# Kernel tuning notes

Hardware: AMD Instinct MI355X
Metric: run time of the kernel (lower is better)

## Reference

```python
import jax, jax.numpy as jnp
import numpy as np
import math

DIM = 1024
D_FF = 1024
B = 128


def setup_inputs() -> dict:
    key = jax.random.key(0)
    ks = jax.random.split(key, 13)
    s = 1.0 / math.sqrt(DIM)
    sf = 1.0 / math.sqrt(D_FF)
    return {
        "x": jax.random.normal(ks[0], (B, DIM), dtype=jnp.float32),
        "Wq": jax.random.uniform(ks[1], (DIM, DIM), jnp.float32, -s, s),
        "bq": jax.random.uniform(ks[2], (DIM,), jnp.float32, -s, s),
        "Wk": jax.random.uniform(ks[3], (DIM, DIM), jnp.float32, -s, s),
        "bk": jax.random.uniform(ks[4], (DIM,), jnp.float32, -s, s),
        "Wv": jax.random.uniform(ks[5], (DIM, DIM), jnp.float32, -s, s),
        "bv": jax.random.uniform(ks[6], (DIM,), jnp.float32, -s, s),
        "Wo": jax.random.uniform(ks[7], (DIM, DIM), jnp.float32, -s, s),
        "bo": jax.random.uniform(ks[8], (DIM,), jnp.float32, -s, s),
        "W1": jax.random.uniform(ks[9], (D_FF, DIM), jnp.float32, -s, s),
        "b1": jax.random.uniform(ks[10], (D_FF,), jnp.float32, -s, s),
        "W2": jax.random.uniform(ks[11], (DIM, D_FF), jnp.float32, -sf, sf),
        "b2": jax.random.uniform(ks[12], (DIM,), jnp.float32, -sf, sf),
    }


def reference(x, Wq, bq, Wk, bk, Wv, bv, Wo, bo, W1, b1, W2, b2):
    # Attention (eval mode: dropout is identity)
    q = x @ Wq.T + bq                      # [B, D]
    k = x @ Wk.T + bk                      # [B, D]
    v = x @ Wv.T + bv                      # [B, D]
    inv_sqrt_dk = 1.0 / math.sqrt(DIM)
    # per-sample outer product: weights[b, i, j] = q[b,i] * k[b,j] / sqrt(d_k)
    weights = (q[:, :, None] * k[:, None, :]) * inv_sqrt_dk  # [B, D, D]
    nw = jax.nn.softmax(weights, axis=-1)                    # [B, D, D]
    attn_out = jnp.einsum('bij,bj->bi', nw, v)               # [B, D]
    attn_out = attn_out @ Wo.T + bo
    # residual 1
    x2 = x + attn_out
    # FFN
    h = jax.nn.relu(x2 @ W1.T + b1)        # [B, d_ff]
    ff = h @ W2.T + b2                     # [B, D]
    out = x2 + ff
    return (out, nw)
```

## Files before the change

### kernel.cpp

```cpp
#include <hip/hip_runtime.h>

#define DIM   1024
#define BATCH 128
#define MAT   (BATCH*DIM)
#define NROWS MAT
#define DS    32

typedef float f4n __attribute__((ext_vector_type(4)));

#define Q_AT  28672
#define A_WO  28672
#define B_WO  47104
#define A_W1  54272
#define B_W1  72704
#define A_W2  79872
#define B_W2  98304
#define MBASE 105472

struct Params {
  const float *x,*Wq,*bq,*Wk,*bk,*Wv,*bv,*Wo,*bo,*W1,*b1,*W2,*b2;
  float *out,*nw;
  float *q,*k,*v,*araw,*x2,*h,*rinv,*P;
};

template<bool USE_RINV>
__device__ __forceinline__ void write_row(const Params& p, int row, int lane)
{
  const int b = row >> 10;
  const float4* __restrict__ k4 = (const float4*)(p.k + ((size_t)b<<10));
  const float4 k0 = k4[lane      ], k1 = k4[lane +  64];
  const float4 k2 = k4[lane + 128], k3 = k4[lane + 192];
  const float c = p.q[row] * 0.03125f;
  f4n* o = (f4n*)(p.nw + ((size_t)row<<10));

  float e[16];
  e[ 0]=__expf(c*k0.x); e[ 1]=__expf(c*k0.y); e[ 2]=__expf(c*k0.z); e[ 3]=__expf(c*k0.w);
  e[ 4]=__expf(c*k1.x); e[ 5]=__expf(c*k1.y); e[ 6]=__expf(c*k1.z); e[ 7]=__expf(c*k1.w);
  e[ 8]=__expf(c*k2.x); e[ 9]=__expf(c*k2.y); e[10]=__expf(c*k2.z); e[11]=__expf(c*k2.w);
  e[12]=__expf(c*k3.x); e[13]=__expf(c*k3.y); e[14]=__expf(c*k3.z); e[15]=__expf(c*k3.w);

  float rinv;
  if (USE_RINV) {
    rinv = p.rinv[row];
  } else {
    float sum = 0.f;
#pragma unroll
    for (int i=0;i<16;++i) sum += e[i];
#pragma unroll
    for (int off=32; off>=1; off>>=1) sum += __shfl_xor(sum, off);
    rinv = 1.f/sum;
  }
#pragma unroll
  for (int t=0;t<4;++t) {
    f4n st;
    st.x = e[4*t+0]*rinv; st.y = e[4*t+1]*rinv;
    st.z = e[4*t+2]*rinv; st.w = e[4*t+3]*rinv;
    __builtin_nontemporal_store(st, &o[lane + 64*t]);
  }
}

template<bool USE_RINV>
__device__ __forceinline__ void write_strided(const Params& p, int w, int NW,
                                              int base, int cap, int lane)
{
#pragma unroll 1
  for (int row = base + w; row < cap; row += NW)
    write_row<USE_RINV>(p, row, lane);
}

__device__ __forceinline__ void ar_rows(const Params& p, int r0, int r1, int lane)
{
  int bcur = -1;
  float4 kr[4], vr[4];
#pragma unroll 1
  for (int row = r0; row < r1; ++row) {
    const int b = row >> 10;
    if (b != bcur) {
      bcur = b;
      const float4* __restrict__ k4 = (const float4*)(p.k + ((size_t)b<<10));
      const float4* __restrict__ v4 = (const float4*)(p.v + ((size_t)b<<10));
#pragma unroll
      for (int t=0;t<4;++t) { kr[t] = k4[lane + 64*t]; vr[t] = v4[lane + 64*t]; }
    }
    const float c = p.q[row] * 0.03125f;
    float sum=0.f, dot=0.f;
#pragma unroll
    for (int t=0;t<4;++t) {
      const float4 kk = kr[t];
      const float4 vv = vr[t];
      float ex = __expf(c*kk.x), ey = __expf(c*kk.y);
      float ez = __expf(c*kk.z), ew = __expf(c*kk.w);
      sum += (ex+ey)+(ez+ew);
      dot += ex*vv.x + ey*vv.y + ez*vv.z + ew*vv.w;
    }
#pragma unroll
    for (int off=32; off>=1; off>>=1) {
      sum += __shfl_xor(sum, off);
      dot += __shfl_xor(dot, off);
    }
    const float rinv = 1.f/sum;
    if (lane==0) { p.araw[row] = dot*rinv; p.rinv[row] = rinv; }
  }
}

__device__ __forceinline__ void gemm_tile(
    const float* __restrict__ X, const float* __restrict__ W,
    float* __restrict__ Pout, int n0, int k0, int KC,
    float* xt, float* wt)
{
  const int tid = threadIdx.x;
  const int tn = tid & 15, tb = tid >> 4;
  const int b_base = tb*8, n_base = tn*4;
  float acc[8][4];
#pragma unroll
  for (int i=0;i<8;++i)
#pragma unroll
    for (int j=0;j<4;++j) acc[i][j]=0.f;

  for (int s=0; s<KC/DS; ++s) {
    const int kk = k0 + s*DS;
#pragma unroll
    for (int r=0;r<4;++r) {
      const int row = (tid>>3) + 32*r;
      const int c0  = (tid&7)*4;
      const float4 vv = *(const float4*)(X + (size_t)row*DIM + kk + c0);
      xt[(c0+0)*132+row]=vv.x; xt[(c0+1)*132+row]=vv.y;
      xt[(c0+2)*132+row]=vv.z; xt[(c0+3)*132+row]=vv.w;
    }
#pragma unroll
    for (int r=0;r<2;++r) {
      const int row = (tid>>3) + 32*r;
      const int c0  = (tid&7)*4;
      const f4n vv = __builtin_nontemporal_load(
          (const f4n*)(W + (size_t)(n0+row)*DIM + kk + c0));
      wt[(c0+0)*68+row]=vv.x; wt[(c0+1)*68+row]=vv.y;
      wt[(c0+2)*68+row]=vv.z; wt[(c0+3)*68+row]=vv.w;
    }
    __syncthreads();
#pragma unroll 4
    for (int d=0; d<DS; ++d) {
      const float4 xa0 = *(const float4*)&xt[d*132 + b_base];
      const float4 xa1 = *(const float4*)&xt[d*132 + b_base + 4];
      const float4 wa  = *(const float4*)&wt[d*68  + n_base];
      const float xr[8] = {xa0.x,xa0.y,xa0.z,xa0.w, xa1.x,xa1.y,xa1.z,xa1.w};
      const float wr[4] = {wa.x,wa.y,wa.z,wa.w};
#pragma unroll
      for (int bb=0;bb<8;++bb)
#pragma unroll
        for (int nn=0;nn<4;++nn) acc[bb][nn] += xr[bb]*wr[nn];
    }
    __syncthreads();
  }
#pragma unroll
  for (int bb=0;bb<8;++bb) {
    const float4 st = make_float4(acc[bb][0],acc[bb][1],acc[bb][2],acc[bb][3]);
    *(float4*)(Pout + (size_t)(b_base+bb)*DIM + n0 + n_base) = st;
  }
}

__global__ __launch_bounds__(256) void qkv_partial(
    const float* __restrict__ X, const float* __restrict__ W0,
    const float* __restrict__ W1, const float* __restrict__ W2,
    float* __restrict__ P)
{
  __shared__ float xt[DS*132];
  __shared__ float wt[DS*68];
  const int z = blockIdx.z;
  const float* W = (z==0)?W0:(z==1)?W1:W2;
  gemm_tile(X, W, P + (size_t)(z*8+blockIdx.y)*MAT,
            blockIdx.x*64, blockIdx.y*128, 128, xt, wt);
}

__global__ __launch_bounds__(256) void qkv_reduce(Params p)
{
  const int t = blockIdx.x*256 + threadIdx.x;
  const int z = t >> 15, idx4 = t & 32767;
  const float4* Pz = (const float4*)(p.P + (size_t)z*8*MAT);
  const float*  bias = (z==0) ? p.bq : (z==1) ? p.bk : p.bv;
  float* outz = (z==0) ? p.q : (z==1) ? p.k : p.v;
  float4 s = Pz[idx4];
#pragma unroll
  for (int sp=1; sp<8; ++sp) {
    const float4 t2 = Pz[sp*(MAT/4)+idx4];
    s.x+=t2.x; s.y+=t2.y; s.z+=t2.z; s.w+=t2.w;
  }
  const float4 b4 = ((const float4*)bias)[idx4 & 255];
  s.x+=b4.x; s.y+=b4.y; s.z+=b4.z; s.w+=b4.w;
  ((float4*)outz)[idx4] = s;
}

__global__ __launch_bounds__(256,4) void attn_mixed(Params p)
{
  const int bid = blockIdx.x, tid = threadIdx.x;
  const int wave = tid>>6, lane = tid&63;
  if (bid < 768) {
    const int gw = bid*4 + wave;
    int r0 = gw*43, r1 = r0 + 43;
    if (r1 > NROWS) r1 = NROWS;
    ar_rows(p, r0, r1, lane);
  } else {
    const int w = (bid-768)*4 + wave;
    write_strided<false>(p, w, 1024, 0, Q_AT, lane);
  }
}

__global__ __launch_bounds__(256,4) void chainA(Params p,
    const float* __restrict__ X, const float* __restrict__ W,
    int wbase, int wcap)
{
  __shared__ float xt[DS*132];
  __shared__ float wt[DS*68];
  const int bid = blockIdx.x, tid = threadIdx.x;
  const int wave = tid>>6, lane = tid&63;
  if (bid < 256) {
    gemm_tile(X, W, p.P + (size_t)(bid&15)*MAT, (bid>>4)*64, (bid&15)*64, 64, xt, wt);
  } else {
    const int w = (bid-256)*4 + wave;
    write_strided<true>(p, w, 3072, wbase, wcap, lane);
  }
}

__global__ __launch_bounds__(256,4) void chainB(Params p,
    const float* __restrict__ bias, const float* __restrict__ extra,
    float* __restrict__ out, int relu, int wbase, int wcap)
{
  const int bid = blockIdx.x, tid = threadIdx.x;
  const int wave = tid>>6, lane = tid&63;
  if (bid < 128) {
    const int idx4 = bid*256 + tid;
    const float4* P4 = (const float4*)p.P;
    float4 s = P4[idx4];
#pragma unroll
    for (int sp=1; sp<16; ++sp) {
      const float4 t2 = P4[sp*(MAT/4)+idx4];
      s.x+=t2.x; s.y+=t2.y; s.z+=t2.z; s.w+=t2.w;
    }
    const float4 b4 = ((const float4*)bias)[idx4 & 255];
    s.x+=b4.x; s.y+=b4.y; s.z+=b4.z; s.w+=b4.w;
    if (relu) { s.x=fmaxf(s.x,0.f); s.y=fmaxf(s.y,0.f);
                s.z=fmaxf(s.z,0.f); s.w=fmaxf(s.w,0.f); }
    if (extra) {
      const float4 e = ((const float4*)extra)[idx4];
      s.x+=e.x; s.y+=e.y; s.z+=e.z; s.w+=e.w;
    }
    ((float4*)out)[idx4] = s;
  } else {
    const int w = (bid-128)*4 + wave;
    write_strided<true>(p, w, 3584, wbase, wcap, lane);
  }
}

__global__ __launch_bounds__(256,4) void mopup(Params p)
{
  const int w = blockIdx.x*4 + (threadIdx.x>>6);
  const int lane = threadIdx.x & 63;
  write_strided<true>(p, w, 4096, MBASE, NROWS, lane);
}

extern "C" void kernel_launch(void* const* d_in, const int* in_sizes, int n_in,
                              void* d_out, int out_size, void* d_ws, size_t ws_size,
                              hipStream_t stream)
{
  (void)in_sizes; (void)n_in; (void)out_size; (void)ws_size;
  Params p;
  p.x  = (const float*)d_in[0];
  p.Wq = (const float*)d_in[1];  p.bq = (const float*)d_in[2];
  p.Wk = (const float*)d_in[3];  p.bk = (const float*)d_in[4];
  p.Wv = (const float*)d_in[5];  p.bv = (const float*)d_in[6];
  p.Wo = (const float*)d_in[7];  p.bo = (const float*)d_in[8];
  p.W1 = (const float*)d_in[9];  p.b1 = (const float*)d_in[10];
  p.W2 = (const float*)d_in[11]; p.b2 = (const float*)d_in[12];
  p.out = (float*)d_out;
  p.nw  = p.out + MAT;
  float* ws = (float*)d_ws;
  p.q    = ws;         p.k    = ws + MAT;   p.v = ws + 2*MAT;
  p.araw = ws + 3*MAT; p.x2   = ws + 4*MAT; p.h = ws + 5*MAT;
  p.rinv = ws + 6*MAT; p.P    = ws + 7*MAT;

  qkv_partial<<<dim3(16,8,3), 256, 0, stream>>>(p.x, p.Wq, p.Wk, p.Wv, p.P);
  qkv_reduce<<<384, 256, 0, stream>>>(p);

  attn_mixed<<<1024, 256, 0, stream>>>(p);

  chainA<<<1024, 256, 0, stream>>>(p, p.araw, p.Wo, A_WO, B_WO);
  chainB<<<1024, 256, 0, stream>>>(p, p.bo, p.x, p.x2, 0, B_WO, A_W1);

  chainA<<<1024, 256, 0, stream>>>(p, p.x2, p.W1, A_W1, B_W1);
  chainB<<<1024, 256, 0, stream>>>(p, p.b1, nullptr, p.h, 1, B_W1, A_W2);

  chainA<<<1024, 256, 0, stream>>>(p, p.h, p.W2, A_W2, B_W2);
  chainB<<<1024, 256, 0, stream>>>(p, p.b2, p.x2, p.out, 0, B_W2, MBASE);

  mopup<<<1024, 256, 0, stream>>>(p);
}
```

Measured before the change: 181.4 us.

## Fuse split-K GEMM and reduction into single per-layer kernel with interleaved softmax writes

Measured after the change: 228.9 us. +26.2%, slower.

```diff
diff --git a/kernel.cpp b/kernel.cpp
--- a/kernel.cpp
+++ b/kernel.cpp
@@ -8,14 +8,9 @@
 
 typedef float f4n __attribute__((ext_vector_type(4)));
 
-#define Q_AT  28672
-#define A_WO  28672
-#define B_WO  47104
-#define A_W1  54272
-#define B_W1  72704
-#define A_W2  79872
-#define B_W2  98304
-#define MBASE 105472
+#define JCAP1 25088
+#define JCAP2 50176
+#define JCAP3 69632
 
 struct Params {
   const float *x,*Wq,*bq,*Wk,*bk,*Wv,*bv,*Wo,*bo,*W1,*b1,*W2,*b2;
@@ -23,7 +18,6 @@
   float *q,*k,*v,*araw,*x2,*h,*rinv,*P;
 };
 
-template<bool USE_RINV>
 __device__ __forceinline__ void write_row(const Params& p, int row, int lane)
 {
   const int b = row >> 10;
@@ -31,76 +25,21 @@
   const float4 k0 = k4[lane      ], k1 = k4[lane +  64];
   const float4 k2 = k4[lane + 128], k3 = k4[lane + 192];
   const float c = p.q[row] * 0.03125f;
+  const float rinv = p.rinv[row];
   f4n* o = (f4n*)(p.nw + ((size_t)row<<10));
-
-  float e[16];
-  e[ 0]=__expf(c*k0.x); e[ 1]=__expf(c*k0.y); e[ 2]=__expf(c*k0.z); e[ 3]=__expf(c*k0.w);
-  e[ 4]=__expf(c*k1.x); e[ 5]=__expf(c*k1.y); e[ 6]=__expf(c*k1.z); e[ 7]=__expf(c*k1.w);
-  e[ 8]=__expf(c*k2.x); e[ 9]=__expf(c*k2.y); e[10]=__expf(c*k2.z); e[11]=__expf(c*k2.w);
-  e[12]=__expf(c*k3.x); e[13]=__expf(c*k3.y); e[14]=__expf(c*k3.z); e[15]=__expf(c*k3.w);
-
-  float rinv;
-  if (USE_RINV) {
-    rinv = p.rinv[row];
-  } else {
-    float sum = 0.f;
-#pragma unroll
-    for (int i=0;i<16;++i) sum += e[i];
-#pragma unroll
-    for (int off=32; off>=1; off>>=1) sum += __shfl_xor(sum, off);
-    rinv = 1.f/sum;
-  }
-#pragma unroll
-  for (int t=0;t<4;++t) {
-    f4n st;
-    st.x = e[4*t+0]*rinv; st.y = e[4*t+1]*rinv;
-    st.z = e[4*t+2]*rinv; st.w = e[4*t+3]*rinv;
-    __builtin_nontemporal_store(st, &o[lane + 64*t]);
-  }
-}
-
-template<bool USE_RINV>
-__device__ __forceinline__ void write_strided(const Params& p, int w, int NW,
-                                              int base, int cap, int lane)
-{
-#pragma unroll 1
-  for (int row = base + w; row < cap; row += NW)
-    write_row<USE_RINV>(p, row, lane);
-}
-
-__device__ __forceinline__ void ar_rows(const Params& p, int r0, int r1, int lane)
-{
-  int bcur = -1;
-  float4 kr[4], vr[4];
-#pragma unroll 1
-  for (int row = r0; row < r1; ++row) {
-    const int b = row >> 10;
-    if (b != bcur) {
-      bcur = b;
-      const float4* __restrict__ k4 = (const float4*)(p.k + ((size_t)b<<10));
-      const float4* __restrict__ v4 = (const float4*)(p.v + ((size_t)b<<10));
-#pragma unroll
-      for (int t=0;t<4;++t) { kr[t] = k4[lane + 64*t]; vr[t] = v4[lane + 64*t]; }
-    }
-    const float c = p.q[row] * 0.03125f;
-    float sum=0.f, dot=0.f;
-#pragma unroll
-    for (int t=0;t<4;++t) {
-      const float4 kk = kr[t];
-      const float4 vv = vr[t];
-      float ex = __expf(c*kk.x), ey = __expf(c*kk.y);
-      float ez = __expf(c*kk.z), ew = __expf(c*kk.w);
-      sum += (ex+ey)+(ez+ew);
-      dot += ex*vv.x + ey*vv.y + ez*vv.z + ew*vv.w;
-    }
-#pragma unroll
-    for (int off=32; off>=1; off>>=1) {
-      sum += __shfl_xor(sum, off);
-      dot += __shfl_xor(dot, off);
-    }
-    const float rinv = 1.f/sum;
-    if (lane==0) { p.araw[row] = dot*rinv; p.rinv[row] = rinv; }
-  }
+  f4n s0, s1, s2, s3;
+  s0.x=__expf(c*k0.x)*rinv; s0.y=__expf(c*k0.y)*rinv;
+  s0.z=__expf(c*k0.z)*rinv; s0.w=__expf(c*k0.w)*rinv;
+  s1.x=__expf(c*k1.x)*rinv; s1.y=__expf(c*k1.y)*rinv;
+  s1.z=__expf(c*k1.z)*rinv; s1.w=__expf(c*k1.w)*rinv;
+  s2.x=__expf(c*k2.x)*rinv; s2.y=__expf(c*k2.y)*rinv;
+  s2.z=__expf(c*k2.z)*rinv; s2.w=__expf(c*k2.w)*rinv;
+  s3.x=__expf(c*k3.x)*rinv; s3.y=__expf(c*k3.y)*rinv;
+  s3.z=__expf(c*k3.z)*rinv; s3.w=__expf(c*k3.w)*rinv;
+  __builtin_nontemporal_store(s0, &o[lane      ]);
+  __builtin_nontemporal_store(s1, &o[lane +  64]);
+  __builtin_nontemporal_store(s2, &o[lane + 128]);
+  __builtin_nontemporal_store(s3, &o[lane + 192]);
 }
 
 __device__ __forceinline__ void gemm_tile(
@@ -189,72 +128,119 @@
   ((float4*)outz)[idx4] = s;
 }
 
-__global__ __launch_bounds__(256,4) void attn_mixed(Params p)
-{
+__global__ __launch_bounds__(256,4) void attn_all(Params p)
+{
+  const int gw = blockIdx.x*4 + (threadIdx.x>>6);
+  const int lane = threadIdx.x & 63;
+  const int b = gw >> 5;
+  const float4* __restrict__ k4 = (const float4*)(p.k + ((size_t)b<<10));
+  const float4* __restrict__ v4 = (const float4*)(p.v + ((size_t)b<<10));
+  float4 kr[4], vr[4];
+#pragma unroll
+  for (int t=0;t<4;++t) { kr[t] = k4[lane + 64*t]; vr[t] = v4[lane + 64*t]; }
+  const int r0 = gw*32;
+#pragma unroll 1
+  for (int r=0;r<32;++r) {
+    const int row = r0 + r;
+    const float c = p.q[row] * 0.03125f;
+    float e[16];
+#pragma unroll
+    for (int t=0;t<4;++t) {
+      e[4*t+0]=__expf(c*kr[t].x); e[4*t+1]=__expf(c*kr[t].y);
+      e[4*t+2]=__expf(c*kr[t].z); e[4*t+3]=__expf(c*kr[t].w);
+    }
+    float sum=0.f, dot=0.f;
+#pragma unroll
+    for (int t=0;t<4;++t) {
+      sum += (e[4*t]+e[4*t+1])+(e[4*t+2]+e[4*t+3]);
+      dot += e[4*t]*vr[t].x + e[4*t+1]*vr[t].y + e[4*t+2]*vr[t].z + e[4*t+3]*vr[t].w;
+    }
+#pragma unroll
+    for (int off=32; off>=1; off>>=1) {
+      sum += __shfl_xor(sum, off);
+      dot += __shfl_xor(dot, off);
+    }
+    const float rinv = 1.f/sum;
+    if (r < 15) {
+      f4n* o = (f4n*)(p.nw + ((size_t)row<<10));
+#pragma unroll
+      for (int t=0;t<4;++t) {
+        f4n st;
+        st.x=e[4*t]*rinv; st.y=e[4*t+1]*rinv;
+        st.z=e[4*t+2]*rinv; st.w=e[4*t+3]*rinv;
+        __builtin_nontemporal_store(st, &o[lane + 64*t]);
+      }
+    }
+    if (lane==0) { p.araw[row] = dot*rinv; p.rinv[row] = rinv; }
+  }
+}
+
+__global__ __launch_bounds__(256,4) void fused_layer(Params p,
+    const float* __restrict__ X, const float* __restrict__ W,
+    const float* __restrict__ bias, const float* __restrict__ extra,
+    float* __restrict__ out, int relu, int jbase, int jcap, int perw)
+{
+  __shared__ float xt[64*132];
+  __shared__ float wt[64*12];
   const int bid = blockIdx.x, tid = threadIdx.x;
   const int wave = tid>>6, lane = tid&63;
-  if (bid < 768) {
-    const int gw = bid*4 + wave;
-    int r0 = gw*43, r1 = r0 + 43;
-    if (r1 > NROWS) r1 = NROWS;
-    ar_rows(p, r0, r1, lane);
-  } else {
-    const int w = (bid-768)*4 + wave;
-    write_strided<false>(p, w, 1024, 0, Q_AT, lane);
-  }
-}
-
-__global__ __launch_bounds__(256,4) void chainA(Params p,
-    const float* __restrict__ X, const float* __restrict__ W,
-    int wbase, int wcap)
-{
-  __shared__ float xt[DS*132];
-  __shared__ float wt[DS*68];
-  const int bid = blockIdx.x, tid = threadIdx.x;
-  const int wave = tid>>6, lane = tid&63;
-  if (bid < 256) {
-    gemm_tile(X, W, p.P + (size_t)(bid&15)*MAT, (bid>>4)*64, (bid&15)*64, 64, xt, wt);
-  } else {
-    const int w = (bid-256)*4 + wave;
-    write_strided<true>(p, w, 3072, wbase, wcap, lane);
-  }
-}
-
-__global__ __launch_bounds__(256,4) void chainB(Params p,
-    const float* __restrict__ bias, const float* __restrict__ extra,
-    float* __restrict__ out, int relu, int wbase, int wcap)
-{
-  const int bid = blockIdx.x, tid = threadIdx.x;
-  const int wave = tid>>6, lane = tid&63;
-  if (bid < 128) {
-    const int idx4 = bid*256 + tid;
-    const float4* P4 = (const float4*)p.P;
-    float4 s = P4[idx4];
-#pragma unroll
-    for (int sp=1; sp<16; ++sp) {
-      const float4 t2 = P4[sp*(MAT/4)+idx4];
-      s.x+=t2.x; s.y+=t2.y; s.z+=t2.z; s.w+=t2.w;
-    }
-    const float4 b4 = ((const float4*)bias)[idx4 & 255];
-    s.x+=b4.x; s.y+=b4.y; s.z+=b4.z; s.w+=b4.w;
-    if (relu) { s.x=fmaxf(s.x,0.f); s.y=fmaxf(s.y,0.f);
-                s.z=fmaxf(s.z,0.f); s.w=fmaxf(s.w,0.f); }
-    if (extra) {
-      const float4 e = ((const float4*)extra)[idx4];
-      s.x+=e.x; s.y+=e.y; s.z+=e.z; s.w+=e.w;
-    }
-    ((float4*)out)[idx4] = s;
-  } else {
+
+  if (bid >= 128) {
     const int w = (bid-128)*4 + wave;
-    write_strided<true>(p, w, 3584, wbase, wcap, lane);
-  }
-}
-
-__global__ __launch_bounds__(256,4) void mopup(Params p)
-{
-  const int w = blockIdx.x*4 + (threadIdx.x>>6);
-  const int lane = threadIdx.x & 63;
-  write_strided<true>(p, w, 4096, MBASE, NROWS, lane);
+    int j = jbase + w*perw;
+#pragma unroll 1
+    for (int i=0;i<perw;++i,++j) {
+      if (j >= jcap) break;
+      const int q17 = j/17, r17 = j - q17*17;
+      write_row(p, q17*32 + 15 + r17, lane);
+    }
+    return;
+  }
+
+  const int n0 = bid*8;
+  const int tb = tid & 31, tn = tid >> 5;
+  const int b0 = tb*4;
+  float acc[4] = {0.f,0.f,0.f,0.f};
+
+  for (int kc=0; kc<DIM; kc+=64) {
+    {
+      const int c0 = (tid&15)*4;
+      const int rb = tid>>4;
+#pragma unroll
+      for (int rr=0;rr<8;++rr) {
+        const int bb = rb + 16*rr;
+        const float4 vv = *(const float4*)(X + (size_t)bb*DIM + kc + c0);
+        xt[(c0+0)*132+bb]=vv.x; xt[(c0+1)*132+bb]=vv.y;
+        xt[(c0+2)*132+bb]=vv.z; xt[(c0+3)*132+bb]=vv.w;
+      }
+    }
+    {
+      const int nn = tid>>5;
+      const int c0 = (tid&31)*2;
+      const float2 vv = *(const float2*)(W + (size_t)(n0+nn)*DIM + kc + c0);
+      wt[(c0+0)*12+nn]=vv.x; wt[(c0+1)*12+nn]=vv.y;
+    }
+    __syncthreads();
+#pragma unroll 8
+    for (int k=0;k<64;++k) {
+      const float4 x4 = *(const float4*)&xt[k*132 + b0];
+      const float  wv = wt[k*12 + tn];
+      acc[0] += x4.x*wv; acc[1] += x4.y*wv;
+      acc[2] += x4.z*wv; acc[3] += x4.w*wv;
+    }
+    __syncthreads();
+  }
+
+  const int col = n0 + tn;
+  const float bv = bias[col];
+#pragma unroll
+  for (int j=0;j<4;++j) {
+    const int bb = b0 + j;
+    float s = acc[j] + bv;
+    if (relu) s = fmaxf(s, 0.f);
+    if (extra) s += extra[(size_t)bb*DIM + col];
+    out[(size_t)bb*DIM + col] = s;
+  }
 }
 
 extern "C" void kernel_launch(void* const* d_in, const int* in_sizes, int n_in,
@@ -280,16 +266,12 @@
   qkv_partial<<<dim3(16,8,3), 256, 0, stream>>>(p.x, p.Wq, p.Wk, p.Wv, p.P);
   qkv_reduce<<<384, 256, 0, stream>>>(p);
 
-  attn_mixed<<<1024, 256, 0, stream>>>(p);
-
-  chainA<<<1024, 256, 0, stream>>>(p, p.araw, p.Wo, A_WO, B_WO);
-  chainB<<<1024, 256, 0, stream>>>(p, p.bo, p.x, p.x2, 0, B_WO, A_W1);
-
-  chainA<<<1024, 256, 0, stream>>>(p, p.x2, p.W1, A_W1, B_W1);
-  chainB<<<1024, 256, 0, stream>>>(p, p.b1, nullptr, p.h, 1, B_W1, A_W2);
-
-  chainA<<<1024, 256, 0, stream>>>(p, p.h, p.W2, A_W2, B_W2);
-  chainB<<<1024, 256, 0, stream>>>(p, p.b2, p.x2, p.out, 0, B_W2, MBASE);
-
-  mopup<<<1024, 256, 0, stream>>>(p);
-}
+  attn_all<<<1024, 256, 0, stream>>>(p);
+
+  fused_layer<<<1024, 256, 0, stream>>>(p, p.araw, p.Wo, p.bo, p.x,
+                                        p.x2, 0, 0,     JCAP1, 7);
+  fused_layer<<<1024, 256, 0, stream>>>(p, p.x2,  p.W1, p.b1, nullptr,
+                                        p.h,  1, JCAP1, JCAP2, 7);
+  fused_layer<<<1024, 256, 0, stream>>>(p, p.h,   p.W2, p.b2, p.x2,
+                                        p.out, 0, JCAP2, JCAP3, 6);
+}
```

## Rebalance nw writes into contiguous per-wave chunks and drop mopup kernel

Applied to the files above, without the earlier changes.

Measured after the change: 227.6 us. 1.25x slower.

```diff
diff --git a/kernel.cpp b/kernel.cpp
--- a/kernel.cpp
+++ b/kernel.cpp
@@ -8,14 +8,12 @@
 
 typedef float f4n __attribute__((ext_vector_type(4)));
 
-#define Q_AT  28672
-#define A_WO  28672
-#define B_WO  47104
-#define A_W1  54272
-#define B_W1  72704
-#define A_W2  79872
-#define B_W2  98304
-#define MBASE 105472
+#define QAT_END 18432
+#define A1_END  46080
+#define B1_END  53248
+#define A2_END  80896
+#define B2_END  88064
+#define A3_END  115712
 
 struct Params {
   const float *x,*Wq,*bq,*Wk,*bk,*Wv,*bv,*Wo,*bo,*W1,*b1,*W2,*b2;
@@ -24,82 +22,45 @@
 };
 
 template<bool USE_RINV>
-__device__ __forceinline__ void write_row(const Params& p, int row, int lane)
-{
-  const int b = row >> 10;
-  const float4* __restrict__ k4 = (const float4*)(p.k + ((size_t)b<<10));
-  const float4 k0 = k4[lane      ], k1 = k4[lane +  64];
-  const float4 k2 = k4[lane + 128], k3 = k4[lane + 192];
-  const float c = p.q[row] * 0.03125f;
-  f4n* o = (f4n*)(p.nw + ((size_t)row<<10));
-
-  float e[16];
-  e[ 0]=__expf(c*k0.x); e[ 1]=__expf(c*k0.y); e[ 2]=__expf(c*k0.z); e[ 3]=__expf(c*k0.w);
-  e[ 4]=__expf(c*k1.x); e[ 5]=__expf(c*k1.y); e[ 6]=__expf(c*k1.z); e[ 7]=__expf(c*k1.w);
-  e[ 8]=__expf(c*k2.x); e[ 9]=__expf(c*k2.y); e[10]=__expf(c*k2.z); e[11]=__expf(c*k2.w);
-  e[12]=__expf(c*k3.x); e[13]=__expf(c*k3.y); e[14]=__expf(c*k3.z); e[15]=__expf(c*k3.w);
-
-  float rinv;
-  if (USE_RINV) {
-    rinv = p.rinv[row];
-  } else {
-    float sum = 0.f;
-#pragma unroll
-    for (int i=0;i<16;++i) sum += e[i];
-#pragma unroll
-    for (int off=32; off>=1; off>>=1) sum += __shfl_xor(sum, off);
-    rinv = 1.f/sum;
-  }
-#pragma unroll
-  for (int t=0;t<4;++t) {
-    f4n st;
-    st.x = e[4*t+0]*rinv; st.y = e[4*t+1]*rinv;
-    st.z = e[4*t+2]*rinv; st.w = e[4*t+3]*rinv;
-    __builtin_nontemporal_store(st, &o[lane + 64*t]);
-  }
-}
-
-template<bool USE_RINV>
-__device__ __forceinline__ void write_strided(const Params& p, int w, int NW,
-                                              int base, int cap, int lane)
-{
-#pragma unroll 1
-  for (int row = base + w; row < cap; row += NW)
-    write_row<USE_RINV>(p, row, lane);
-}
-
-__device__ __forceinline__ void ar_rows(const Params& p, int r0, int r1, int lane)
+__device__ __forceinline__ void write_chunk(const Params& p, int r0, int r1, int lane)
 {
   int bcur = -1;
-  float4 kr[4], vr[4];
+  float4 kr[4];
 #pragma unroll 1
   for (int row = r0; row < r1; ++row) {
     const int b = row >> 10;
     if (b != bcur) {
       bcur = b;
       const float4* __restrict__ k4 = (const float4*)(p.k + ((size_t)b<<10));
-      const float4* __restrict__ v4 = (const float4*)(p.v + ((size_t)b<<10));
-#pragma unroll
-      for (int t=0;t<4;++t) { kr[t] = k4[lane + 64*t]; vr[t] = v4[lane + 64*t]; }
+#pragma unroll
+      for (int t=0;t<4;++t) kr[t] = k4[lane + 64*t];
     }
     const float c = p.q[row] * 0.03125f;
-    float sum=0.f, dot=0.f;
+    float e[16];
 #pragma unroll
     for (int t=0;t<4;++t) {
-      const float4 kk = kr[t];
-      const float4 vv = vr[t];
-      float ex = __expf(c*kk.x), ey = __expf(c*kk.y);
-      float ez = __expf(c*kk.z), ew = __expf(c*kk.w);
-      sum += (ex+ey)+(ez+ew);
-      dot += ex*vv.x + ey*vv.y + ez*vv.z + ew*vv.w;
-    }
-#pragma unroll
-    for (int off=32; off>=1; off>>=1) {
-      sum += __shfl_xor(sum, off);
-      dot += __shfl_xor(dot, off);
-    }
-    const float rinv = 1.f/sum;
-    if (lane==0) { p.araw[row] = dot*rinv; p.rinv[row] = rinv; }
+      e[4*t+0]=__expf(c*kr[t].x); e[4*t+1]=__expf(c*kr[t].y);
+      e[4*t+2]=__expf(c*kr[t].z); e[4*t+3]=__expf(c*kr[t].w);
+    }
+    float rinv;
+    if (USE_RINV) {
+      rinv = p.rinv[row];
+    } else {
+      float sum = 0.f;
+#pragma unroll
+      for (int i=0;i<16;++i) sum += e[i];
+#pragma unroll
+      for (int off=32; off>=1; off>>=1) sum += __shfl_xor(sum, off);
+      rinv = 1.f/sum;
+    }
+    f4n* o = (f4n*)(p.nw + ((size_t)row<<10));
+#pragma unroll
+    for (int t=0;t<4;++t) {
+      f4n st;
+      st.x=e[4*t]*rinv;   st.y=e[4*t+1]*rinv;
+      st.z=e[4*t+2]*rinv; st.w=e[4*t+3]*rinv;
+      __builtin_nontemporal_store(st, &o[lane + 64*t]);
+    }
   }
 }
 
@@ -193,20 +154,43 @@
 {
   const int bid = blockIdx.x, tid = threadIdx.x;
   const int wave = tid>>6, lane = tid&63;
-  if (bid < 768) {
+  if (bid < 256) {
     const int gw = bid*4 + wave;
-    int r0 = gw*43, r1 = r0 + 43;
-    if (r1 > NROWS) r1 = NROWS;
-    ar_rows(p, r0, r1, lane);
+    const int b = gw >> 3;
+    const float4* __restrict__ k4 = (const float4*)(p.k + ((size_t)b<<10));
+    const float4* __restrict__ v4 = (const float4*)(p.v + ((size_t)b<<10));
+    float4 kr[4], vr[4];
+#pragma unroll
+    for (int t=0;t<4;++t) { kr[t] = k4[lane + 64*t]; vr[t] = v4[lane + 64*t]; }
+    const int r0 = gw*128;
+#pragma unroll 1
+    for (int r=0;r<128;++r) {
+      const int row = r0 + r;
+      const float c = p.q[row] * 0.03125f;
+      float sum=0.f, dot=0.f;
+#pragma unroll
+      for (int t=0;t<4;++t) {
+        const float ex=__expf(c*kr[t].x), ey=__expf(c*kr[t].y);
+        const float ez=__expf(c*kr[t].z), ew=__expf(c*kr[t].w);
+        sum += (ex+ey)+(ez+ew);
+        dot += ex*vr[t].x + ey*vr[t].y + ez*vr[t].z + ew*vr[t].w;
+      }
+#pragma unroll
+      for (int off=32; off>=1; off>>=1) {
+        sum += __shfl_xor(sum, off);
+        dot += __shfl_xor(dot, off);
+      }
+      const float rinv = 1.f/sum;
+      if (lane==0) { p.araw[row] = dot*rinv; p.rinv[row] = rinv; }
+    }
   } else {
-    const int w = (bid-768)*4 + wave;
-    write_strided<false>(p, w, 1024, 0, Q_AT, lane);
+    const int w = (bid-256)*4 + wave;
+    write_chunk<false>(p, w*6, w*6 + 6, lane);
   }
 }
 
 __global__ __launch_bounds__(256,4) void chainA(Params p,
-    const float* __restrict__ X, const float* __restrict__ W,
-    int wbase, int wcap)
+    const float* __restrict__ X, const float* __restrict__ W, int wbase)
 {
   __shared__ float xt[DS*132];
   __shared__ float wt[DS*68];
@@ -216,13 +200,14 @@
     gemm_tile(X, W, p.P + (size_t)(bid&15)*MAT, (bid>>4)*64, (bid&15)*64, 64, xt, wt);
   } else {
     const int w = (bid-256)*4 + wave;
-    write_strided<true>(p, w, 3072, wbase, wcap, lane);
+    const int r0 = wbase + w*9;
+    write_chunk<true>(p, r0, r0 + 9, lane);
   }
 }
 
 __global__ __launch_bounds__(256,4) void chainB(Params p,
     const float* __restrict__ bias, const float* __restrict__ extra,
-    float* __restrict__ out, int relu, int wbase, int wcap)
+    float* __restrict__ out, int relu, int wbase, int last)
 {
   const int bid = blockIdx.x, tid = threadIdx.x;
   const int wave = tid>>6, lane = tid&63;
@@ -246,15 +231,16 @@
     ((float4*)out)[idx4] = s;
   } else {
     const int w = (bid-128)*4 + wave;
-    write_strided<true>(p, w, 3584, wbase, wcap, lane);
-  }
-}
-
-__global__ __launch_bounds__(256,4) void mopup(Params p)
-{
-  const int w = blockIdx.x*4 + (threadIdx.x>>6);
-  const int lane = threadIdx.x & 63;
-  write_strided<true>(p, w, 4096, MBASE, NROWS, lane);
+    if (!last) {
+      const int r0 = wbase + w*2;
+      write_chunk<true>(p, r0, r0 + 2, lane);
+    } else {
+      int r0, n;
+      if (w < 1024) { r0 = wbase + w*5;            n = 5; }
+      else          { r0 = wbase + 5120 + (w-1024)*4; n = 4; }
+      write_chunk<true>(p, r0, r0 + n, lane);
+    }
+  }
 }
 
 extern "C" void kernel_launch(void* const* d_in, const int* in_sizes, int n_in,
@@ -282,14 +268,12 @@
 
   attn_mixed<<<1024, 256, 0, stream>>>(p);
 
-  chainA<<<1024, 256, 0, stream>>>(p, p.araw, p.Wo, A_WO, B_WO);
-  chainB<<<1024, 256, 0, stream>>>(p, p.bo, p.x, p.x2, 0, B_WO, A_W1);
-
-  chainA<<<1024, 256, 0, stream>>>(p, p.x2, p.W1, A_W1, B_W1);
-  chainB<<<1024, 256, 0, stream>>>(p, p.b1, nullptr, p.h, 1, B_W1, A_W2);
-
-  chainA<<<1024, 256, 0, stream>>>(p, p.h, p.W2, A_W2, B_W2);
-  chainB<<<1024, 256, 0, stream>>>(p, p.b2, p.x2, p.out, 0, B_W2, MBASE);
-
-  mopup<<<1024, 256, 0, stream>>>(p);
-}
+  chainA<<<1024, 256, 0, stream>>>(p, p.araw, p.Wo, QAT_END);
+  chainB<<<1024, 256, 0, stream>>>(p, p.bo, p.x, p.x2, 0, A1_END, 0);
+
+  chainA<<<1024, 256, 0, stream>>>(p, p.x2, p.W1, B1_END);
+  chainB<<<1024, 256, 0, stream>>>(p, p.b1, nullptr, p.h, 1, A2_END, 0);
+
+  chainA<<<1024, 256, 0, stream>>>(p, p.h, p.W2, B2_END);
+  chainB<<<1024, 256, 0, stream>>>(p, p.b2, p.x2, p.out, 0, A3_END, 1);
+}
```
